# Performance work log

Hardware: AMD Instinct MI355X
Metric: run time of the kernel (lower is better)

## Reference

```python
import jax, jax.numpy as jnp
import numpy as np

H = 16        # attn_num
A = 64        # head dim
W = 512       # sliding-window length (ar_attn_window_len)
THETA = 10000.0
EPS = 1e-6    # norm_eps


def _rope(x):
    # x: [b, h, s, a]
    s, a = x.shape[2], x.shape[3]
    inv_freq = (1.0 / THETA) ** (jnp.arange(0, a, 2, dtype=jnp.float32) / a)
    freqs = jnp.arange(s, dtype=jnp.float32)[:, None] * inv_freq[None, :]  # [s, a/2]
    cos, sin = jnp.cos(freqs), jnp.sin(freqs)
    x1, x2 = jnp.split(x, 2, axis=-1)
    return jnp.concatenate([x1 * cos + x2 * sin, -x1 * sin + x2 * cos], axis=-1)


def _l2_normalize(x):
    # F.normalize(x, dim=-1, eps): x / max(||x||_2, eps)
    n = jnp.sqrt(jnp.sum(x * x, axis=-1, keepdims=True))
    return x / jnp.maximum(n, EPS)


def setup_inputs() -> dict:
    key = jax.random.key(0)
    kq, kk, kv = jax.random.split(key, 3)
    b, s, d = 2, 4096, H * A
    return {
        "xq": jax.random.normal(kq, (b, s, d), dtype=jnp.float32),
        "xk": jax.random.normal(kk, (b, s, d), dtype=jnp.float32),
        "xv": jax.random.normal(kv, (b, s, d), dtype=jnp.float32),
    }


def reference(xq, xk, xv):
    b, s, d = xq.shape
    to_heads = lambda x: x.reshape(b, s, H, A).transpose(0, 2, 1, 3)  # b h s a
    q, k, v = to_heads(xq), to_heads(xk), to_heads(xv)

    # qk-norm then RoPE, exactly as Attention.forward
    q = _rope(_l2_normalize(q))
    k = _rope(_l2_normalize(k))

    # Block-banded causal sliding-window attention (honors the block sparsity):
    # query block i attends only to key blocks i-1 and i (window = block size W).
    nb = s // W
    qb = q.reshape(b, H, nb, W, A)

    def band(x):
        xb = x.reshape(b, H, nb, W, A)
        xp = jnp.pad(xb, ((0, 0), (0, 0), (1, 0), (0, 0), (0, 0)))  # zero block in front
        return jnp.concatenate([xp[:, :, :-1], xp[:, :, 1:]], axis=3)  # [b,H,nb,2W,A]

    kb, vb = band(k), band(v)

    scale = 1.0 / np.sqrt(A)
    scores = jnp.einsum("bhnqa,bhnka->bhnqk", qb, kb) * scale  # [b,H,nb,W,2W]

    # mask: causal (q >= kv), window (q - kv < W), and kv index in range (>= 0)
    r = jnp.arange(W)
    c = jnp.arange(2 * W)
    diff = r[:, None] - (c[None, :] - W)               # q_global - kv_global
    within = (diff >= 0) & (diff < W)                   # [W, 2W]
    kv_global = (jnp.arange(nb)[:, None] - 1) * W + c[None, :]  # [nb, 2W]
    mask = within[None, :, :] & (kv_global[:, None, :] >= 0)    # [nb, W, 2W]

    scores = jnp.where(mask[None, None], scores, -1e30)
    p = jax.nn.softmax(scores, axis=-1)
    out = jnp.einsum("bhnqk,bhnka->bhnqa", p, vb)       # [b,H,nb,W,A]
    out = out.reshape(b, H, s, A).transpose(0, 2, 1, 3).reshape(b, s, d)
    return out
```

## Files before the change

### kernel.cpp

```cpp
#include <hip/hip_runtime.h>

#define NB 2
#define NH 16
#define SEQ 4096
#define HD 64
#define DIM 1024
#define WIN 512

typedef float f32x16 __attribute__((ext_vector_type(16)));
typedef short bf16x8 __attribute__((ext_vector_type(8)));
typedef unsigned int u32x4 __attribute__((ext_vector_type(4)));
typedef unsigned int u32x2 __attribute__((ext_vector_type(2)));
typedef unsigned short u16;
typedef unsigned int u32;

__device__ __forceinline__ u16 f2bf(float x) {
    u32 u = __float_as_uint(x);
    u += 0x7FFFu + ((u >> 16) & 1u);
    return (u16)(u >> 16);
}

__device__ __forceinline__ u32 cvtpk(float lo, float hi) {
    u32 r;
    asm("v_cvt_pk_bf16_f32 %0, %1, %2" : "=v"(r) : "v"(lo), "v"(hi));
    return r;
}

__device__ __forceinline__ float pexp2(float x) {
    return 1.f + x * (0.69314718f + x * 0.24022651f);
}

__device__ __forceinline__ void norm_rope_row2(const float* __restrict__ row,
                                               const float (&cr)[8], const float (&sr)[8],
                                               float scale, u16* __restrict__ dst, int a) {
    float4 u0 = *(const float4*)(row + 8 * a);
    float4 u1 = *(const float4*)(row + 8 * a + 4);
    float4 v0 = *(const float4*)(row + 32 + 8 * a);
    float4 v1 = *(const float4*)(row + 32 + 8 * a + 4);
    float x1[8] = {u0.x, u0.y, u0.z, u0.w, u1.x, u1.y, u1.z, u1.w};
    float x2[8] = {v0.x, v0.y, v0.z, v0.w, v1.x, v1.y, v1.z, v1.w};
    float ss = 0.f;
#pragma unroll
    for (int i = 0; i < 8; ++i) ss += x1[i] * x1[i] + x2[i] * x2[i];
    ss += __shfl_xor(ss, 1);
    ss += __shfl_xor(ss, 2);
    float rn = scale / fmaxf(sqrtf(ss), 1e-6f);
    u16 o1[8], o2[8];
#pragma unroll
    for (int i = 0; i < 8; ++i) {
        float c = cr[i], sn = sr[i];
        o1[i] = f2bf((x1[i] * c + x2[i] * sn) * rn);
        o2[i] = f2bf((x2[i] * c - x1[i] * sn) * rn);
    }
    uint4 w1, w2;
    w1.x = (u32)o1[0] | ((u32)o1[1] << 16); w1.y = (u32)o1[2] | ((u32)o1[3] << 16);
    w1.z = (u32)o1[4] | ((u32)o1[5] << 16); w1.w = (u32)o1[6] | ((u32)o1[7] << 16);
    w2.x = (u32)o2[0] | ((u32)o2[1] << 16); w2.y = (u32)o2[2] | ((u32)o2[3] << 16);
    w2.z = (u32)o2[4] | ((u32)o2[5] << 16); w2.w = (u32)o2[6] | ((u32)o2[7] << 16);
    *(uint4*)(dst + 8 * a) = w1;
    *(uint4*)(dst + 32 + 8 * a) = w2;
}

__global__ void kv_prep(const float* __restrict__ xk, const float* __restrict__ xv,
                        float* __restrict__ ctab, float* __restrict__ stab,
                        u16* __restrict__ Kn, u16* __restrict__ Vt) {
    __shared__ u16 tile[64][66];
    int bid = blockIdx.x;
    int t = threadIdx.x;
    if (bid < 2048) {
        int bh = bid >> 6, stile = bid & 63;
        int b = bh >> 4, h = bh & 15;
        int lr = t >> 2, a = t & 3;
        int s = stile * 64 + lr;
        float c8[8], s8[8];
#pragma unroll
        for (int i = 0; i < 8; ++i) {
            float invf = exp2f((float)(8 * a + i) * -0.4152410118f);
            float ang = (float)s * invf;
            c8[i] = cosf(ang);
            s8[i] = sinf(ang);
        }
        size_t inoff = ((size_t)(b * SEQ + s)) * DIM + h * HD;
        size_t outoff = ((size_t)bh * SEQ + s) * HD;
        norm_rope_row2(xk + inoff, c8, s8, 1.0f, Kn + outoff, a);
    } else if (bid < 4096) {
        int vb = bid - 2048;
        int bh = vb >> 6, stile = vb & 63;
        int b = bh >> 4, h = bh & 15;
        int lr = t >> 2, a = t & 3;
        int s = stile * 64 + lr;
        const float* vrow = xv + ((size_t)(b * SEQ + s)) * DIM + h * HD + 16 * a;
#pragma unroll
        for (int c = 0; c < 4; ++c) {
            float4 w = *(const float4*)(vrow + 4 * c);
            tile[lr][16 * a + 4 * c + 0] = f2bf(w.x);
            tile[lr][16 * a + 4 * c + 1] = f2bf(w.y);
            tile[lr][16 * a + 4 * c + 2] = f2bf(w.z);
            tile[lr][16 * a + 4 * c + 3] = f2bf(w.w);
        }
        __syncthreads();
        int d = t >> 2;
        u32 pk[8];
#pragma unroll
        for (int i = 0; i < 8; ++i) {
            u16 lo = tile[16 * a + 2 * i][d];
            u16 hi = tile[16 * a + 2 * i + 1][d];
            pk[i] = (u32)lo | ((u32)hi << 16);
        }
        u16* dst = Vt + ((size_t)bh * HD + d) * SEQ + stile * 64 + 16 * a;
        *(uint4*)(dst) = make_uint4(pk[0], pk[1], pk[2], pk[3]);
        *(uint4*)(dst + 8) = make_uint4(pk[4], pk[5], pk[6], pk[7]);
    } else {
        int idx = (bid - 4096) * 256 + t;
        int s = idx >> 5, j = idx & 31;
        float invf = exp2f((float)j * -0.4152410118f);
        float ang = (float)s * invf;
        ctab[idx] = cosf(ang);
        stab[idx] = sinf(ang);
    }
}

#define KROW 72
#define VROW 40
__global__ __launch_bounds__(256, 4) void attn_kernel(const float* __restrict__ xq,
                                                      const u16* __restrict__ Kn,
                                                      const u16* __restrict__ Vt,
                                                      const float* __restrict__ ctab,
                                                      const float* __restrict__ stab,
                                                      float* __restrict__ out) {
    __shared__ __align__(16) u16 Kl[2][32 * KROW];
    __shared__ __align__(16) u16 Vl[2][64 * VROW];
    int phys = blockIdx.x;
    int logical = (phys & 7) * 128 + (phys >> 3);
    int bh = logical >> 5, qt = logical & 31;
    int b = bh >> 4, h = bh & 15;
    int tid = threadIdx.x;
    int w = tid >> 6, l = tid & 63;
    int q = l & 31, hi = l >> 5;
    int qblk = qt * 128;
    int qw0 = qblk + w * 32;
    const u16* Kh = Kn + (size_t)bh * SEQ * HD;
    const u16* Vh = Vt + (size_t)bh * HD * SEQ;
    int dq = qw0 + q;

    int bt0 = (qblk - (WIN - 1)) >> 5; if (bt0 < 0) bt0 = 0;
    int bt1 = (qblk + 96) >> 5;

    int krow = tid >> 3, kc = (tid & 7) * 8;
    int vrw  = tid >> 2, vc = (tid & 3) * 8;
    const u16* kgl = Kh + (size_t)krow * HD + kc;
    const u16* vgl = Vh + (size_t)vrw * SEQ + vc;
    u16* kls0 = &Kl[0][krow * KROW + kc];
    u16* kls1 = &Kl[1][krow * KROW + kc];
    u16* vls0 = &Vl[0][vrw * VROW + vc];
    u16* vls1 = &Vl[1][vrw * VROW + vc];

    {
        uint4 gk = *(const uint4*)(kgl + ((size_t)bt0 << 5) * HD);
        uint4 gv = *(const uint4*)(vgl + (bt0 << 5));
        *(uint4*)kls0 = gk;
        *(uint4*)vls0 = gv;
    }

    const float* qrow = xq + ((size_t)(b * SEQ + dq)) * DIM + h * HD;
    float4 xa0 = *(const float4*)(qrow + hi * 8);
    float4 xa1 = *(const float4*)(qrow + hi * 8 + 4);
    float4 xb0 = *(const float4*)(qrow + 16 + hi * 8);
    float4 xb1 = *(const float4*)(qrow + 16 + hi * 8 + 4);
    float4 ya0 = *(const float4*)(qrow + 32 + hi * 8);
    float4 ya1 = *(const float4*)(qrow + 36 + hi * 8);
    float4 yb0 = *(const float4*)(qrow + 48 + hi * 8);
    float4 yb1 = *(const float4*)(qrow + 52 + hi * 8);
    auto d4 = [](float4 v) { return v.x * v.x + v.y * v.y + v.z * v.z + v.w * v.w; };
    float ss = d4(xa0) + d4(xa1) + d4(xb0) + d4(xb1) + d4(ya0) + d4(ya1) + d4(yb0) + d4(yb1);
    ss += __shfl_xor(ss, 32);
    float rn = (0.125f * 1.44269504f) / fmaxf(sqrtf(ss), 1e-6f);
    const float* crp = ctab + (size_t)dq * 32;
    const float* srp = stab + (size_t)dq * 32;
    float4 ca0 = *(const float4*)(crp + hi * 8);
    float4 ca1 = *(const float4*)(crp + hi * 8 + 4);
    float4 cb0 = *(const float4*)(crp + 16 + hi * 8);
    float4 cb1 = *(const float4*)(crp + 16 + hi * 8 + 4);
    float4 sa0 = *(const float4*)(srp + hi * 8);
    float4 sa1 = *(const float4*)(srp + hi * 8 + 4);
    float4 sb0 = *(const float4*)(srp + 16 + hi * 8);
    float4 sb1 = *(const float4*)(srp + 16 + hi * 8 + 4);
    auto mk1 = [&](float4 x0, float4 x1f, float4 y0, float4 y1f,
                   float4 c0, float4 c1, float4 s0, float4 s1) -> bf16x8 {
        u32x4 r;
        r[0] = cvtpk((x0.x * c0.x + y0.x * s0.x) * rn, (x0.y * c0.y + y0.y * s0.y) * rn);
        r[1] = cvtpk((x0.z * c0.z + y0.z * s0.z) * rn, (x0.w * c0.w + y0.w * s0.w) * rn);
        r[2] = cvtpk((x1f.x * c1.x + y1f.x * s1.x) * rn, (x1f.y * c1.y + y1f.y * s1.y) * rn);
        r[3] = cvtpk((x1f.z * c1.z + y1f.z * s1.z) * rn, (x1f.w * c1.w + y1f.w * s1.w) * rn);
        return __builtin_bit_cast(bf16x8, r);
    };
    auto mk2 = [&](float4 x0, float4 x1f, float4 y0, float4 y1f,
                   float4 c0, float4 c1, float4 s0, float4 s1) -> bf16x8 {
        u32x4 r;
        r[0] = cvtpk((y0.x * c0.x - x0.x * s0.x) * rn, (y0.y * c0.y - x0.y * s0.y) * rn);
        r[1] = cvtpk((y0.z * c0.z - x0.z * s0.z) * rn, (y0.w * c0.w - x0.w * s0.w) * rn);
        r[2] = cvtpk((y1f.x * c1.x - x1f.x * s1.x) * rn, (y1f.y * c1.y - x1f.y * s1.y) * rn);
        r[3] = cvtpk((y1f.z * c1.z - x1f.z * s1.z) * rn, (y1f.w * c1.w - x1f.w * s1.w) * rn);
        return __builtin_bit_cast(bf16x8, r);
    };
    bf16x8 qf0 = mk1(xa0, xa1, ya0, ya1, ca0, ca1, sa0, sa1);
    bf16x8 qf1 = mk1(xb0, xb1, yb0, yb1, cb0, cb1, sb0, sb1);
    bf16x8 qf2 = mk2(xa0, xa1, ya0, ya1, ca0, ca1, sa0, sa1);
    bf16x8 qf3 = mk2(xb0, xb1, yb0, yb1, cb0, cb1, sb0, sb1);

    f32x16 acc0, acc1;
#pragma unroll
    for (int i = 0; i < 16; ++i) { acc0[i] = 0.f; acc1[i] = 0.f; }
    float l_ = 0.f;

    int tw0 = (qw0 - (WIN - 1)) >> 5; if (tw0 < 0) tw0 = 0;
    int tw1 = qw0 >> 5;

    const u16* krd0 = &Kl[0][q * KROW + hi * 8];
    const u16* krd1 = &Kl[1][q * KROW + hi * 8];
    const u16* vrd0a = &Vl[0][q * VROW + hi * 8];
    const u16* vrd0b = &Vl[0][(32 + q) * VROW + hi * 8];
    const u16* vrd1a = &Vl[1][q * VROW + hi * 8];
    const u16* vrd1b = &Vl[1][(32 + q) * VROW + hi * 8];

    __syncthreads();

    int c = 0;
    for (int t = bt0; t <= bt1; ++t) {
        int kv0 = t << 5;
        bool more = t < bt1;
        uint4 gk, gv;
        if (more) {
            gk = *(const uint4*)(kgl + ((size_t)(kv0 + 32)) * HD);
            gv = *(const uint4*)(vgl + (kv0 + 32));
        }
        __builtin_amdgcn_sched_barrier(0);

        if (t >= tw0 && t <= tw1) {
            bool mask = (t == tw0) || (t == tw1);
            const u16* kr = c ? krd1 : krd0;
            const u16* va = c ? vrd1a : vrd0a;
            const u16* vb = c ? vrd1b : vrd0b;

            bf16x8 k0 = *(const bf16x8*)(kr);
            bf16x8 k1 = *(const bf16x8*)(kr + 16);
            bf16x8 k2 = *(const bf16x8*)(kr + 32);
            bf16x8 k3 = *(const bf16x8*)(kr + 48);

            f32x16 st;
#pragma unroll
            for (int i = 0; i < 16; ++i) st[i] = 0.f;
            __builtin_amdgcn_s_setprio(1);
            st = __builtin_amdgcn_mfma_f32_32x32x16_bf16(k0, qf0, st, 0, 0, 0);
            st = __builtin_amdgcn_mfma_f32_32x32x16_bf16(k1, qf1, st, 0, 0, 0);
            st = __builtin_amdgcn_mfma_f32_32x32x16_bf16(k2, qf2, st, 0, 0, 0);
            st = __builtin_amdgcn_mfma_f32_32x32x16_bf16(k3, qf3, st, 0, 0, 0);
            __builtin_amdgcn_s_setprio(0);

            bf16x8 va0 = *(const bf16x8*)(va);
            bf16x8 va1 = *(const bf16x8*)(va + 16);
            bf16x8 vb0 = *(const bf16x8*)(vb);
            bf16x8 vb1 = *(const bf16x8*)(vb + 16);

            int base = dq - (kv0 + 4 * hi);
            u32 wd[8];
            float l0 = 0.f, l1 = 0.f;
#pragma unroll
            for (int i = 0; i < 8; ++i) {
                int r0 = 2 * i, r1 = 2 * i + 1;
                float e0 = pexp2(st[r0]);
                float e1 = pexp2(st[r1]);
                if (mask) {
                    int k0off = (r0 & 3) + 8 * (r0 >> 2);
                    int k1off = (r1 & 3) + 8 * (r1 >> 2);
                    e0 = ((u32)(base - k0off) < (u32)WIN) ? e0 : 0.f;
                    e1 = ((u32)(base - k1off) < (u32)WIN) ? e1 : 0.f;
                }
                l0 += e0; l1 += e1;
                wd[i] = cvtpk(e0, e1);
            }
            l_ += l0 + l1;

            u32x4 b1, b2;
#if __has_builtin(__builtin_amdgcn_permlane32_swap)
            u32x2 sA = __builtin_amdgcn_permlane32_swap(wd[0], wd[2], false, false);
            u32x2 sB = __builtin_amdgcn_permlane32_swap(wd[1], wd[3], false, false);
            u32x2 sC = __builtin_amdgcn_permlane32_swap(wd[4], wd[6], false, false);
            u32x2 sD = __builtin_amdgcn_permlane32_swap(wd[5], wd[7], false, false);
            b1 = (u32x4){ sA[0], sB[0], sA[1], sB[1] };
            b2 = (u32x4){ sC[0], sD[0], sC[1], sD[1] };
#else
            u32 e0 = __shfl_xor(hi ? wd[0] : wd[2], 32);
            u32 e1 = __shfl_xor(hi ? wd[1] : wd[3], 32);
            u32 e2 = __shfl_xor(hi ? wd[4] : wd[6], 32);
            u32 e3 = __shfl_xor(hi ? wd[5] : wd[7], 32);
            b1 = (u32x4){ hi ? e0 : wd[0], hi ? e1 : wd[1], hi ? wd[2] : e0, hi ? wd[3] : e1 };
            b2 = (u32x4){ hi ? e2 : wd[4], hi ? e3 : wd[5], hi ? wd[6] : e2, hi ? wd[7] : e3 };
#endif
            bf16x8 pb1 = __builtin_bit_cast(bf16x8, b1);
            bf16x8 pb2 = __builtin_bit_cast(bf16x8, b2);

            __builtin_amdgcn_s_setprio(1);
            acc0 = __builtin_amdgcn_mfma_f32_32x32x16_bf16(va0, pb1, acc0, 0, 0, 0);
            acc0 = __builtin_amdgcn_mfma_f32_32x32x16_bf16(va1, pb2, acc0, 0, 0, 0);
            acc1 = __builtin_amdgcn_mfma_f32_32x32x16_bf16(vb0, pb1, acc1, 0, 0, 0);
            acc1 = __builtin_amdgcn_mfma_f32_32x32x16_bf16(vb1, pb2, acc1, 0, 0, 0);
            __builtin_amdgcn_s_setprio(0);
        }

        if (more) {
            *(uint4*)(c ? kls0 : kls1) = gk;
            *(uint4*)(c ? vls0 : vls1) = gv;
            __syncthreads();
        }
        c ^= 1;
    }

    l_ += __shfl_xor(l_, 32);
    float inv = 1.0f / l_;
    float* orow = out + ((size_t)(b * SEQ + dq)) * DIM + h * HD;
#pragma unroll
    for (int g = 0; g < 4; ++g) {
        float4 v0 = { acc0[4 * g + 0] * inv, acc0[4 * g + 1] * inv,
                      acc0[4 * g + 2] * inv, acc0[4 * g + 3] * inv };
        float4 v1 = { acc1[4 * g + 0] * inv, acc1[4 * g + 1] * inv,
                      acc1[4 * g + 2] * inv, acc1[4 * g + 3] * inv };
        *(float4*)(orow + 8 * g + 4 * hi) = v0;
        *(float4*)(orow + 32 + 8 * g + 4 * hi) = v1;
    }
}

extern "C" void kernel_launch(void* const* d_in, const int* in_sizes, int n_in,
                              void* d_out, int out_size, void* d_ws, size_t ws_size,
                              hipStream_t stream) {
    (void)in_sizes; (void)n_in; (void)out_size; (void)ws_size;
    const float* xq = (const float*)d_in[0];
    const float* xk = (const float*)d_in[1];
    const float* xv = (const float*)d_in[2];
    float* out = (float*)d_out;

    const size_t HEADS_ELEMS = (size_t)NB * NH * SEQ * HD;
    u16* Kn = (u16*)d_ws;
    u16* Vt = Kn + HEADS_ELEMS;
    float* ctab = (float*)(Vt + HEADS_ELEMS);
    float* stab = ctab + (size_t)SEQ * 32;

    kv_prep<<<dim3(4608), dim3(256), 0, stream>>>(xk, xv, ctab, stab, Kn, Vt);
    attn_kernel<<<dim3(1024), dim3(256), 0, stream>>>(xq, Kn, Vt, ctab, stab, out);
}
```

Measured before the change: 61.12 us.

## Process two 32-query sub-tiles per wave to reuse K/V tiles

Each block now covers 256 queries and each wave handles 64 queries as two 32-row sub-tiles, computing separate score and PV MFMAs against the same K/V fragments read from LDS. The grid is halved and launch bounds lowered to 2 blocks per CU. This amortises K/V global and LDS loads across more queries, at the cost of more registers, fewer waves in flight, and longer per-block loops.

New measurement: 71.46 us. +16.9%, slower.

```diff
diff --git a/kernel.cpp b/kernel.cpp
--- a/kernel.cpp
+++ b/kernel.cpp
@@ -122,7 +122,7 @@
 
 #define KROW 72
 #define VROW 40
-__global__ __launch_bounds__(256, 4) void attn_kernel(const float* __restrict__ xq,
+__global__ __launch_bounds__(256, 2) void attn_kernel(const float* __restrict__ xq,
                                                       const u16* __restrict__ Kn,
                                                       const u16* __restrict__ Vt,
                                                       const float* __restrict__ ctab,
@@ -131,20 +131,21 @@
     __shared__ __align__(16) u16 Kl[2][32 * KROW];
     __shared__ __align__(16) u16 Vl[2][64 * VROW];
     int phys = blockIdx.x;
-    int logical = (phys & 7) * 128 + (phys >> 3);
-    int bh = logical >> 5, qt = logical & 31;
+    int logical = (phys & 7) * 64 + (phys >> 3);
+    int bh = logical >> 4, qt = logical & 15;
     int b = bh >> 4, h = bh & 15;
     int tid = threadIdx.x;
     int w = tid >> 6, l = tid & 63;
     int q = l & 31, hi = l >> 5;
-    int qblk = qt * 128;
-    int qw0 = qblk + w * 32;
+    int qblk = qt * 256;
+    int qw0 = qblk + w * 64;
     const u16* Kh = Kn + (size_t)bh * SEQ * HD;
     const u16* Vh = Vt + (size_t)bh * HD * SEQ;
-    int dq = qw0 + q;
+    int dqA = qw0 + q;
+    int dqB = dqA + 32;
 
     int bt0 = (qblk - (WIN - 1)) >> 5; if (bt0 < 0) bt0 = 0;
-    int bt1 = (qblk + 96) >> 5;
+    int bt1 = (qblk + 224) >> 5;
 
     int krow = tid >> 3, kc = (tid & 7) * 8;
     int vrw  = tid >> 2, vc = (tid & 3) * 8;
@@ -162,59 +163,65 @@
         *(uint4*)vls0 = gv;
     }
 
-    const float* qrow = xq + ((size_t)(b * SEQ + dq)) * DIM + h * HD;
-    float4 xa0 = *(const float4*)(qrow + hi * 8);
-    float4 xa1 = *(const float4*)(qrow + hi * 8 + 4);
-    float4 xb0 = *(const float4*)(qrow + 16 + hi * 8);
-    float4 xb1 = *(const float4*)(qrow + 16 + hi * 8 + 4);
-    float4 ya0 = *(const float4*)(qrow + 32 + hi * 8);
-    float4 ya1 = *(const float4*)(qrow + 36 + hi * 8);
-    float4 yb0 = *(const float4*)(qrow + 48 + hi * 8);
-    float4 yb1 = *(const float4*)(qrow + 52 + hi * 8);
-    auto d4 = [](float4 v) { return v.x * v.x + v.y * v.y + v.z * v.z + v.w * v.w; };
-    float ss = d4(xa0) + d4(xa1) + d4(xb0) + d4(xb1) + d4(ya0) + d4(ya1) + d4(yb0) + d4(yb1);
-    ss += __shfl_xor(ss, 32);
-    float rn = (0.125f * 1.44269504f) / fmaxf(sqrtf(ss), 1e-6f);
-    const float* crp = ctab + (size_t)dq * 32;
-    const float* srp = stab + (size_t)dq * 32;
-    float4 ca0 = *(const float4*)(crp + hi * 8);
-    float4 ca1 = *(const float4*)(crp + hi * 8 + 4);
-    float4 cb0 = *(const float4*)(crp + 16 + hi * 8);
-    float4 cb1 = *(const float4*)(crp + 16 + hi * 8 + 4);
-    float4 sa0 = *(const float4*)(srp + hi * 8);
-    float4 sa1 = *(const float4*)(srp + hi * 8 + 4);
-    float4 sb0 = *(const float4*)(srp + 16 + hi * 8);
-    float4 sb1 = *(const float4*)(srp + 16 + hi * 8 + 4);
-    auto mk1 = [&](float4 x0, float4 x1f, float4 y0, float4 y1f,
-                   float4 c0, float4 c1, float4 s0, float4 s1) -> bf16x8 {
+    auto makeQ = [&](int dq, bf16x8& f0, bf16x8& f1, bf16x8& f2, bf16x8& f3) {
+        const float* qrow = xq + ((size_t)(b * SEQ + dq)) * DIM + h * HD;
+        float4 xa0 = *(const float4*)(qrow + hi * 8);
+        float4 xa1 = *(const float4*)(qrow + hi * 8 + 4);
+        float4 xb0 = *(const float4*)(qrow + 16 + hi * 8);
+        float4 xb1 = *(const float4*)(qrow + 16 + hi * 8 + 4);
+        float4 ya0 = *(const float4*)(qrow + 32 + hi * 8);
+        float4 ya1 = *(const float4*)(qrow + 36 + hi * 8);
+        float4 yb0 = *(const float4*)(qrow + 48 + hi * 8);
+        float4 yb1 = *(const float4*)(qrow + 52 + hi * 8);
+        auto d4 = [](float4 v) { return v.x * v.x + v.y * v.y + v.z * v.z + v.w * v.w; };
+        float ss = d4(xa0) + d4(xa1) + d4(xb0) + d4(xb1) + d4(ya0) + d4(ya1) + d4(yb0) + d4(yb1);
+        ss += __shfl_xor(ss, 32);
+        float rn = (0.125f * 1.44269504f) / fmaxf(sqrtf(ss), 1e-6f);
+        const float* crp = ctab + (size_t)dq * 32;
+        const float* srp = stab + (size_t)dq * 32;
+        float4 ca0 = *(const float4*)(crp + hi * 8);
+        float4 ca1 = *(const float4*)(crp + hi * 8 + 4);
+        float4 cb0 = *(const float4*)(crp + 16 + hi * 8);
+        float4 cb1 = *(const float4*)(crp + 16 + hi * 8 + 4);
+        float4 sa0 = *(const float4*)(srp + hi * 8);
+        float4 sa1 = *(const float4*)(srp + hi * 8 + 4);
+        float4 sb0 = *(const float4*)(srp + 16 + hi * 8);
+        float4 sb1 = *(const float4*)(srp + 16 + hi * 8 + 4);
         u32x4 r;
-        r[0] = cvtpk((x0.x * c0.x + y0.x * s0.x) * rn, (x0.y * c0.y + y0.y * s0.y) * rn);
-        r[1] = cvtpk((x0.z * c0.z + y0.z * s0.z) * rn, (x0.w * c0.w + y0.w * s0.w) * rn);
-        r[2] = cvtpk((x1f.x * c1.x + y1f.x * s1.x) * rn, (x1f.y * c1.y + y1f.y * s1.y) * rn);
-        r[3] = cvtpk((x1f.z * c1.z + y1f.z * s1.z) * rn, (x1f.w * c1.w + y1f.w * s1.w) * rn);
-        return __builtin_bit_cast(bf16x8, r);
+        r[0] = cvtpk((xa0.x * ca0.x + ya0.x * sa0.x) * rn, (xa0.y * ca0.y + ya0.y * sa0.y) * rn);
+        r[1] = cvtpk((xa0.z * ca0.z + ya0.z * sa0.z) * rn, (xa0.w * ca0.w + ya0.w * sa0.w) * rn);
+        r[2] = cvtpk((xa1.x * ca1.x + ya1.x * sa1.x) * rn, (xa1.y * ca1.y + ya1.y * sa1.y) * rn);
+        r[3] = cvtpk((xa1.z * ca1.z + ya1.z * sa1.z) * rn, (xa1.w * ca1.w + ya1.w * sa1.w) * rn);
+        f0 = __builtin_bit_cast(bf16x8, r);
+        r[0] = cvtpk((xb0.x * cb0.x + yb0.x * sb0.x) * rn, (xb0.y * cb0.y + yb0.y * sb0.y) * rn);
+        r[1] = cvtpk((xb0.z * cb0.z + yb0.z * sb0.z) * rn, (xb0.w * cb0.w + yb0.w * sb0.w) * rn);
+        r[2] = cvtpk((xb1.x * cb1.x + yb1.x * sb1.x) * rn, (xb1.y * cb1.y + yb1.y * sb1.y) * rn);
+        r[3] = cvtpk((xb1.z * cb1.z + yb1.z * sb1.z) * rn, (xb1.w * cb1.w + yb1.w * sb1.w) * rn);
+        f1 = __builtin_bit_cast(bf16x8, r);
+        r[0] = cvtpk((ya0.x * ca0.x - xa0.x * sa0.x) * rn, (ya0.y * ca0.y - xa0.y * sa0.y) * rn);
+        r[1] = cvtpk((ya0.z * ca0.z - xa0.z * sa0.z) * rn, (ya0.w * ca0.w - xa0.w * sa0.w) * rn);
+        r[2] = cvtpk((ya1.x * ca1.x - xa1.x * sa1.x) * rn, (ya1.y * ca1.y - xa1.y * sa1.y) * rn);
+        r[3] = cvtpk((ya1.z * ca1.z - xa1.z * sa1.z) * rn, (ya1.w * ca1.w - xa1.w * sa1.w) * rn);
+        f2 = __builtin_bit_cast(bf16x8, r);
+        r[0] = cvtpk((yb0.x * cb0.x - xb0.x * sb0.x) * rn, (yb0.y * cb0.y - xb0.y * sb0.y) * rn);
+        r[1] = cvtpk((yb0.z * cb0.z - xb0.z * sb0.z) * rn, (yb0.w * cb0.w - xb0.w * sb0.w) * rn);
+        r[2] = cvtpk((yb1.x * cb1.x - xb1.x * sb1.x) * rn, (yb1.y * cb1.y - xb1.y * sb1.y) * rn);
+        r[3] = cvtpk((yb1.z * cb1.z - xb1.z * sb1.z) * rn, (yb1.w * cb1.w - xb1.w * sb1.w) * rn);
+        f3 = __builtin_bit_cast(bf16x8, r);
     };
-    auto mk2 = [&](float4 x0, float4 x1f, float4 y0, float4 y1f,
-                   float4 c0, float4 c1, float4 s0, float4 s1) -> bf16x8 {
-        u32x4 r;
-        r[0] = cvtpk((y0.x * c0.x - x0.x * s0.x) * rn, (y0.y * c0.y - x0.y * s0.y) * rn);
-        r[1] = cvtpk((y0.z * c0.z - x0.z * s0.z) * rn, (y0.w * c0.w - x0.w * s0.w) * rn);
-        r[2] = cvtpk((y1f.x * c1.x - x1f.x * s1.x) * rn, (y1f.y * c1.y - x1f.y * s1.y) * rn);
-        r[3] = cvtpk((y1f.z * c1.z - x1f.z * s1.z) * rn, (y1f.w * c1.w - x1f.w * s1.w) * rn);
-        return __builtin_bit_cast(bf16x8, r);
-    };
-    bf16x8 qf0 = mk1(xa0, xa1, ya0, ya1, ca0, ca1, sa0, sa1);
-    bf16x8 qf1 = mk1(xb0, xb1, yb0, yb1, cb0, cb1, sb0, sb1);
-    bf16x8 qf2 = mk2(xa0, xa1, ya0, ya1, ca0, ca1, sa0, sa1);
-    bf16x8 qf3 = mk2(xb0, xb1, yb0, yb1, cb0, cb1, sb0, sb1);
-
-    f32x16 acc0, acc1;
-#pragma unroll
-    for (int i = 0; i < 16; ++i) { acc0[i] = 0.f; acc1[i] = 0.f; }
-    float l_ = 0.f;
-
-    int tw0 = (qw0 - (WIN - 1)) >> 5; if (tw0 < 0) tw0 = 0;
-    int tw1 = qw0 >> 5;
+    bf16x8 qfA0, qfA1, qfA2, qfA3, qfB0, qfB1, qfB2, qfB3;
+    makeQ(dqA, qfA0, qfA1, qfA2, qfA3);
+    makeQ(dqB, qfB0, qfB1, qfB2, qfB3);
+
+    f32x16 accA0, accA1, accB0, accB1;
+#pragma unroll
+    for (int i = 0; i < 16; ++i) { accA0[i] = 0.f; accA1[i] = 0.f; accB0[i] = 0.f; accB1[i] = 0.f; }
+    float lA = 0.f, lB = 0.f;
+
+    int twA0 = (qw0 - (WIN - 1)) >> 5; if (twA0 < 0) twA0 = 0;
+    int twA1 = qw0 >> 5;
+    int twB0 = (qw0 + 32 - (WIN - 1)) >> 5; if (twB0 < 0) twB0 = 0;
+    int twB1 = (qw0 + 32) >> 5;
 
     const u16* krd0 = &Kl[0][q * KROW + hi * 8];
     const u16* krd1 = &Kl[1][q * KROW + hi * 8];
@@ -236,76 +243,90 @@
         }
         __builtin_amdgcn_sched_barrier(0);
 
-        if (t >= tw0 && t <= tw1) {
-            bool mask = (t == tw0) || (t == tw1);
+        bool inA = (t >= twA0) && (t <= twA1);
+        bool inB = (t >= twB0) && (t <= twB1);
+        if (inA || inB) {
             const u16* kr = c ? krd1 : krd0;
-            const u16* va = c ? vrd1a : vrd0a;
-            const u16* vb = c ? vrd1b : vrd0b;
-
             bf16x8 k0 = *(const bf16x8*)(kr);
             bf16x8 k1 = *(const bf16x8*)(kr + 16);
             bf16x8 k2 = *(const bf16x8*)(kr + 32);
             bf16x8 k3 = *(const bf16x8*)(kr + 48);
 
-            f32x16 st;
-#pragma unroll
-            for (int i = 0; i < 16; ++i) st[i] = 0.f;
+            f32x16 stA, stB;
             __builtin_amdgcn_s_setprio(1);
-            st = __builtin_amdgcn_mfma_f32_32x32x16_bf16(k0, qf0, st, 0, 0, 0);
-            st = __builtin_amdgcn_mfma_f32_32x32x16_bf16(k1, qf1, st, 0, 0, 0);
-            st = __builtin_amdgcn_mfma_f32_32x32x16_bf16(k2, qf2, st, 0, 0, 0);
-            st = __builtin_amdgcn_mfma_f32_32x32x16_bf16(k3, qf3, st, 0, 0, 0);
+            if (inA) {
+#pragma unroll
+                for (int i = 0; i < 16; ++i) stA[i] = 0.f;
+                stA = __builtin_amdgcn_mfma_f32_32x32x16_bf16(k0, qfA0, stA, 0, 0, 0);
+                stA = __builtin_amdgcn_mfma_f32_32x32x16_bf16(k1, qfA1, stA, 0, 0, 0);
+                stA = __builtin_amdgcn_mfma_f32_32x32x16_bf16(k2, qfA2, stA, 0, 0, 0);
+                stA = __builtin_amdgcn_mfma_f32_32x32x16_bf16(k3, qfA3, stA, 0, 0, 0);
+            }
+            if (inB) {
+#pragma unroll
+                for (int i = 0; i < 16; ++i) stB[i] = 0.f;
+                stB = __builtin_amdgcn_mfma_f32_32x32x16_bf16(k0, qfB0, stB, 0, 0, 0);
+                stB = __builtin_amdgcn_mfma_f32_32x32x16_bf16(k1, qfB1, stB, 0, 0, 0);
+                stB = __builtin_amdgcn_mfma_f32_32x32x16_bf16(k2, qfB2, stB, 0, 0, 0);
+                stB = __builtin_amdgcn_mfma_f32_32x32x16_bf16(k3, qfB3, stB, 0, 0, 0);
+            }
             __builtin_amdgcn_s_setprio(0);
 
+            const u16* va = c ? vrd1a : vrd0a;
+            const u16* vb = c ? vrd1b : vrd0b;
             bf16x8 va0 = *(const bf16x8*)(va);
             bf16x8 va1 = *(const bf16x8*)(va + 16);
             bf16x8 vb0 = *(const bf16x8*)(vb);
             bf16x8 vb1 = *(const bf16x8*)(vb + 16);
 
-            int base = dq - (kv0 + 4 * hi);
-            u32 wd[8];
-            float l0 = 0.f, l1 = 0.f;
-#pragma unroll
-            for (int i = 0; i < 8; ++i) {
-                int r0 = 2 * i, r1 = 2 * i + 1;
-                float e0 = pexp2(st[r0]);
-                float e1 = pexp2(st[r1]);
-                if (mask) {
-                    int k0off = (r0 & 3) + 8 * (r0 >> 2);
-                    int k1off = (r1 & 3) + 8 * (r1 >> 2);
-                    e0 = ((u32)(base - k0off) < (u32)WIN) ? e0 : 0.f;
-                    e1 = ((u32)(base - k1off) < (u32)WIN) ? e1 : 0.f;
+            auto smpv = [&](const f32x16& st, int dq, bool mask,
+                            f32x16& a0, f32x16& a1, float& lsum) {
+                int base = dq - (kv0 + 4 * hi);
+                u32 wd[8];
+                float l0 = 0.f, l1 = 0.f;
+#pragma unroll
+                for (int i = 0; i < 8; ++i) {
+                    int r0 = 2 * i, r1 = 2 * i + 1;
+                    float e0 = pexp2(st[r0]);
+                    float e1 = pexp2(st[r1]);
+                    if (mask) {
+                        int k0off = (r0 & 3) + 8 * (r0 >> 2);
+                        int k1off = (r1 & 3) + 8 * (r1 >> 2);
+                        e0 = ((u32)(base - k0off) < (u32)WIN) ? e0 : 0.f;
+                        e1 = ((u32)(base - k1off) < (u32)WIN) ? e1 : 0.f;
+                    }
+                    l0 += e0; l1 += e1;
+                    wd[i] = cvtpk(e0, e1);
                 }
-                l0 += e0; l1 += e1;
-                wd[i] = cvtpk(e0, e1);
-            }
-            l_ += l0 + l1;
-
-            u32x4 b1, b2;
+                lsum += l0 + l1;
+                u32x4 b1, b2;
 #if __has_builtin(__builtin_amdgcn_permlane32_swap)
-            u32x2 sA = __builtin_amdgcn_permlane32_swap(wd[0], wd[2], false, false);
-            u32x2 sB = __builtin_amdgcn_permlane32_swap(wd[1], wd[3], false, false);
-            u32x2 sC = __builtin_amdgcn_permlane32_swap(wd[4], wd[6], false, false);
-            u32x2 sD = __builtin_amdgcn_permlane32_swap(wd[5], wd[7], false, false);
-            b1 = (u32x4){ sA[0], sB[0], sA[1], sB[1] };
-            b2 = (u32x4){ sC[0], sD[0], sC[1], sD[1] };
+                u32x2 sA = __builtin_amdgcn_permlane32_swap(wd[0], wd[2], false, false);
+                u32x2 sB = __builtin_amdgcn_permlane32_swap(wd[1], wd[3], false, false);
+                u32x2 sC = __builtin_amdgcn_permlane32_swap(wd[4], wd[6], false, false);
+                u32x2 sD = __builtin_amdgcn_permlane32_swap(wd[5], wd[7], false, false);
+                b1 = (u32x4){ sA[0], sB[0], sA[1], sB[1] };
+                b2 = (u32x4){ sC[0], sD[0], sC[1], sD[1] };
 #else
-            u32 e0 = __shfl_xor(hi ? wd[0] : wd[2], 32);
-            u32 e1 = __shfl_xor(hi ? wd[1] : wd[3], 32);
-            u32 e2 = __shfl_xor(hi ? wd[4] : wd[6], 32);
-            u32 e3 = __shfl_xor(hi ? wd[5] : wd[7], 32);
-            b1 = (u32x4){ hi ? e0 : wd[0], hi ? e1 : wd[1], hi ? wd[2] : e0, hi ? wd[3] : e1 };
-            b2 = (u32x4){ hi ? e2 : wd[4], hi ? e3 : wd[5], hi ? wd[6] : e2, hi ? wd[7] : e3 };
+                u32 e0 = __shfl_xor(hi ? wd[0] : wd[2], 32);
+                u32 e1 = __shfl_xor(hi ? wd[1] : wd[3], 32);
+                u32 e2 = __shfl_xor(hi ? wd[4] : wd[6], 32);
+                u32 e3 = __shfl_xor(hi ? wd[5] : wd[7], 32);
+                b1 = (u32x4){ hi ? e0 : wd[0], hi ? e1 : wd[1], hi ? wd[2] : e0, hi ? wd[3] : e1 };
+                b2 = (u32x4){ hi ? e2 : wd[4], hi ? e3 : wd[5], hi ? wd[6] : e2, hi ? wd[7] : e3 };
 #endif
-            bf16x8 pb1 = __builtin_bit_cast(bf16x8, b1);
-            bf16x8 pb2 = __builtin_bit_cast(bf16x8, b2);
-
-            __builtin_amdgcn_s_setprio(1);
-            acc0 = __builtin_amdgcn_mfma_f32_32x32x16_bf16(va0, pb1, acc0, 0, 0, 0);
-            acc0 = __builtin_amdgcn_mfma_f32_32x32x16_bf16(va1, pb2, acc0, 0, 0, 0);
-            acc1 = __builtin_amdgcn_mfma_f32_32x32x16_bf16(vb0, pb1, acc1, 0, 0, 0);
-            acc1 = __builtin_amdgcn_mfma_f32_32x32x16_bf16(vb1, pb2, acc1, 0, 0, 0);
-            __builtin_amdgcn_s_setprio(0);
+                bf16x8 pb1 = __builtin_bit_cast(bf16x8, b1);
+                bf16x8 pb2 = __builtin_bit_cast(bf16x8, b2);
+                __builtin_amdgcn_s_setprio(1);
+                a0 = __builtin_amdgcn_mfma_f32_32x32x16_bf16(va0, pb1, a0, 0, 0, 0);
+                a0 = __builtin_amdgcn_mfma_f32_32x32x16_bf16(va1, pb2, a0, 0, 0, 0);
+                a1 = __builtin_amdgcn_mfma_f32_32x32x16_bf16(vb0, pb1, a1, 0, 0, 0);
+                a1 = __builtin_amdgcn_mfma_f32_32x32x16_bf16(vb1, pb2, a1, 0, 0, 0);
+                __builtin_amdgcn_s_setprio(0);
+            };
+
+            if (inA) smpv(stA, dqA, (t == twA0) || (t == twA1), accA0, accA1, lA);
+            if (inB) smpv(stB, dqB, (t == twB0) || (t == twB1), accB0, accB1, lB);
         }
 
         if (more) {
@@ -316,17 +337,26 @@
         c ^= 1;
     }
 
-    l_ += __shfl_xor(l_, 32);
-    float inv = 1.0f / l_;
-    float* orow = out + ((size_t)(b * SEQ + dq)) * DIM + h * HD;
+    lA += __shfl_xor(lA, 32);
+    lB += __shfl_xor(lB, 32);
+    float invA = 1.0f / lA;
+    float invB = 1.0f / lB;
+    float* orowA = out + ((size_t)(b * SEQ + dqA)) * DIM + h * HD;
+    float* orowB = out + ((size_t)(b * SEQ + dqB)) * DIM + h * HD;
 #pragma unroll
     for (int g = 0; g < 4; ++g) {
-        float4 v0 = { acc0[4 * g + 0] * inv, acc0[4 * g + 1] * inv,
-                      acc0[4 * g + 2] * inv, acc0[4 * g + 3] * inv };
-        float4 v1 = { acc1[4 * g + 0] * inv, acc1[4 * g + 1] * inv,
-                      acc1[4 * g + 2] * inv, acc1[4 * g + 3] * inv };
-        *(float4*)(orow + 8 * g + 4 * hi) = v0;
-        *(float4*)(orow + 32 + 8 * g + 4 * hi) = v1;
+        float4 v0 = { accA0[4 * g + 0] * invA, accA0[4 * g + 1] * invA,
+                      accA0[4 * g + 2] * invA, accA0[4 * g + 3] * invA };
+        float4 v1 = { accA1[4 * g + 0] * invA, accA1[4 * g + 1] * invA,
+                      accA1[4 * g + 2] * invA, accA1[4 * g + 3] * invA };
+        *(float4*)(orowA + 8 * g + 4 * hi) = v0;
+        *(float4*)(orowA + 32 + 8 * g + 4 * hi) = v1;
+        float4 w0 = { accB0[4 * g + 0] * invB, accB0[4 * g + 1] * invB,
+                      accB0[4 * g + 2] * invB, accB0[4 * g + 3] * invB };
+        float4 w1 = { accB1[4 * g + 0] * invB, accB1[4 * g + 1] * invB,
+                      accB1[4 * g + 2] * invB, accB1[4 * g + 3] * invB };
+        *(float4*)(orowB + 8 * g + 4 * hi) = w0;
+        *(float4*)(orowB + 32 + 8 * g + 4 * hi) = w1;
     }
 }
 
@@ -346,5 +376,5 @@
     float* stab = ctab + (size_t)SEQ * 32;
 
     kv_prep<<<dim3(4608), dim3(256), 0, stream>>>(xk, xv, ctab, stab, Kn, Vt);
-    attn_kernel<<<dim3(1024), dim3(256), 0, stream>>>(xq, Kn, Vt, ctab, stab, out);
-}
+    attn_kernel<<<dim3(512), dim3(256), 0, stream>>>(xq, Kn, Vt, ctab, stab, out);
+}
```
